# Kernel tuning notes

Measured on AMD Instinct MI355X. Metric: run time of the kernel, lower is better.

## Reference

```python
import jax, jax.numpy as jnp
import numpy as np

F, H, C = 768, 256, 16  # feature_size, lstm_hidden_size, num_classes
B, T = 256, 128         # sentences per doc, words per sentence


def lstm_scan(x, w_ih, w_hh, b, reverse=False):
    """PyTorch-convention LSTM (gates i,f,g,o). x: [B,T,D] -> (outputs [B,T,H], h_T [B,H])."""
    Hh = w_hh.shape[1]
    gx = jnp.einsum('btd,gd->btg', x, w_ih) + b      # [B,T,4H], biases fused
    gx = jnp.swapaxes(gx, 0, 1)                      # [T,B,4H]
    h0 = jnp.zeros((x.shape[0], Hh), x.dtype)
    def step(carry, g):
        h, c = carry
        g = g + h @ w_hh.T
        i, f, gg, o = jnp.split(g, 4, axis=-1)
        c = jax.nn.sigmoid(f) * c + jax.nn.sigmoid(i) * jnp.tanh(gg)
        h = jax.nn.sigmoid(o) * jnp.tanh(c)
        return (h, c), h
    (hT, _), ys = jax.lax.scan(step, (h0, h0), gx, reverse=reverse)
    return jnp.swapaxes(ys, 0, 1), hT


def setup_inputs() -> dict:
    key = jax.random.key(0)
    ks = jax.random.split(key, 16)
    s = 0.1
    return {
        'x': jax.random.normal(ks[0], (B, T, F), jnp.float32),
        'y': jax.random.randint(ks[1], (B,), 0, C),
        'mask': jnp.ones((B, T), bool),
        # BiLSTM forward / reverse directions
        'w_ih_f': jax.random.normal(ks[2], (4 * H, F)) * s,
        'w_hh_f': jax.random.normal(ks[3], (4 * H, H)) * s,
        'b_f': jax.random.normal(ks[4], (4 * H,)) * s,
        'w_ih_r': jax.random.normal(ks[5], (4 * H, F)) * s,
        'w_hh_r': jax.random.normal(ks[6], (4 * H, H)) * s,
        'b_r': jax.random.normal(ks[7], (4 * H,)) * s,
        # word_to_sent LSTM (512 -> 512)
        'w_ih_s': jax.random.normal(ks[8], (8 * H, 2 * H)) * s,
        'w_hh_s': jax.random.normal(ks[9], (8 * H, 2 * H)) * s,
        'b_s': jax.random.normal(ks[10], (8 * H,)) * s,
        # linear + CRF params
        'lin_w': jax.random.normal(ks[11], (C, 2 * H)) * s,
        'lin_b': jnp.zeros((C,)),
        'crf_start': jax.random.normal(ks[12], (C,)) * s,
        'crf_end': jax.random.normal(ks[13], (C,)) * s,
        'crf_trans': jax.random.normal(ks[14], (C, C)) * s,
    }


def reference(x, y, mask, w_ih_f, w_hh_f, b_f, w_ih_r, w_hh_r, b_r,
              w_ih_s, w_hh_s, b_s, lin_w, lin_b, crf_start, crf_end, crf_trans):
    # dropout is identity (eval-mode reference)
    out_f, _ = lstm_scan(x, w_ih_f, w_hh_f, b_f, reverse=False)
    out_r, _ = lstm_scan(x, w_ih_r, w_hh_r, b_r, reverse=True)
    h = jnp.concatenate([out_f, out_r], axis=-1)          # [B,T,2H]
    _, hT = lstm_scan(h, w_ih_s, w_hh_s, b_s)             # [B,2H] final hidden per sentence
    emissions = hT @ lin_w.T + lin_b                      # [B,C] -> CRF sequence of length B

    S = emissions.shape[0]
    # numerator: score of gold tag sequence
    num = (crf_start[y[0]] + emissions[jnp.arange(S), y].sum()
           + crf_trans[y[:-1], y[1:]].sum() + crf_end[y[-1]])
    # denominator: forward algorithm (log partition)
    def fstep(alpha, e_t):
        return jax.nn.logsumexp(alpha[:, None] + crf_trans + e_t[None, :], axis=0), None
    alpha0 = crf_start + emissions[0]
    alphaT, _ = jax.lax.scan(fstep, alpha0, emissions[1:])
    denom = jax.nn.logsumexp(alphaT + crf_end)
    return num - denom  # log-likelihood (sum reduction, single CRF batch)
```

## Files before the change

kernel.cpp:

```cpp
#include <hip/hip_runtime.h>
#include <hip/hip_bf16.h>
#include <stdint.h>


typedef __bf16 bf16_t;
typedef __bf16 bf16x8 __attribute__((ext_vector_type(8)));
typedef __bf16 bf16x4v __attribute__((ext_vector_type(4)));
typedef float f32x4 __attribute__((ext_vector_type(4)));
typedef unsigned long long u64;

#define MFMA_BF16(a, b, c) __builtin_amdgcn_mfma_f32_16x16x32_bf16((a), (b), (c), 0, 0, 0)

__device__ __forceinline__ float sigm_(float x) { return 1.f / (1.f + __expf(-x)); }
__device__ __forceinline__ float tanh_(float x) {
  x = fminf(20.f, fmaxf(-20.f, x));
  float e = __expf(-2.f * x);
  return (1.f - e) / (1.f + e);
}

__device__ __forceinline__ u64 aload8(const u64* p) {
  return __hip_atomic_load(p, __ATOMIC_RELAXED, __HIP_MEMORY_SCOPE_AGENT);
}
__device__ __forceinline__ void astore8(u64* p, u64 v) {
  __hip_atomic_store(p, v, __ATOMIC_RELAXED, __HIP_MEMORY_SCOPE_AGENT);
}

union U8 { bf16x4v v; uint2 u; };
union B8 { uint32_t u[4]; bf16x8 v; };

__global__ void zero8(u64* __restrict__ p, int n) {
  int i = blockIdx.x * 256 + threadIdx.x;
  int s = gridDim.x * 256;
  for (; i < n; i += s) p[i] = 0ull;
}

__global__ void cvt4(const float* __restrict__ in, bf16_t* __restrict__ out, int n4) {
  int i = blockIdx.x * blockDim.x + threadIdx.x;
  int stride = gridDim.x * blockDim.x;
  for (; i < n4; i += stride) {
    float4 v = ((const float4*)in)[i];
    bf16x4v o;
    o.x = (bf16_t)v.x; o.y = (bf16_t)v.y; o.z = (bf16_t)v.z; o.w = (bf16_t)v.w;
    ((bf16x4v*)out)[i] = o;
  }
}

__global__ void __launch_bounds__(256, 2)
gemm_bt(const bf16_t* __restrict__ A, const bf16_t* __restrict__ B,
        bf16_t* __restrict__ C, int M, int N, int K) {
  const int tid = threadIdx.x;
  const int w = tid >> 6, lane = tid & 63, quad = lane >> 4, l15 = lane & 15;
  const int ntiles = N >> 7;
  const int m0 = (blockIdx.x / ntiles) << 7;
  const int n0 = (blockIdx.x % ntiles) << 7;
  const int wm = (w >> 1) << 6, wn = (w & 1) << 6;

  __shared__ bf16_t As[128 * 72];
  __shared__ bf16_t Bs[128 * 72];

  const f32x4 z4 = {0.f, 0.f, 0.f, 0.f};
  f32x4 acc[4][4];
#pragma unroll
  for (int i = 0; i < 4; ++i)
#pragma unroll
    for (int j = 0; j < 4; ++j) acc[i][j] = z4;

  const int nk = K >> 6;
  for (int kt = 0; kt < nk; ++kt) {
    uint4 av[4], bv[4];
#pragma unroll
    for (int i = 0; i < 4; ++i) {
      int cid = tid + i * 256;
      int r = cid >> 3, c = cid & 7;
      av[i] = *(const uint4*)&A[(size_t)(m0 + r) * K + kt * 64 + c * 8];
      bv[i] = *(const uint4*)&B[(size_t)(n0 + r) * K + kt * 64 + c * 8];
    }
    __syncthreads();
#pragma unroll
    for (int i = 0; i < 4; ++i) {
      int cid = tid + i * 256;
      int r = cid >> 3, c = cid & 7;
      *(uint4*)&As[r * 72 + c * 8] = av[i];
      *(uint4*)&Bs[r * 72 + c * 8] = bv[i];
    }
    __syncthreads();
#pragma unroll
    for (int s = 0; s < 2; ++s) {
      bf16x8 af[4], bfr[4];
#pragma unroll
      for (int i = 0; i < 4; ++i)
        af[i] = *(const bf16x8*)&As[(wm + i * 16 + l15) * 72 + s * 32 + quad * 8];
#pragma unroll
      for (int j = 0; j < 4; ++j)
        bfr[j] = *(const bf16x8*)&Bs[(wn + j * 16 + l15) * 72 + s * 32 + quad * 8];
#pragma unroll
      for (int i = 0; i < 4; ++i)
#pragma unroll
        for (int j = 0; j < 4; ++j)
          acc[i][j] = MFMA_BF16(af[i], bfr[j], acc[i][j]);
    }
  }
#pragma unroll
  for (int i = 0; i < 4; ++i)
#pragma unroll
    for (int j = 0; j < 4; ++j)
#pragma unroll
      for (int p = 0; p < 4; ++p) {
        int row = m0 + wm + i * 16 + quad * 4 + p;
        int col = n0 + wn + j * 16 + l15;
        C[(size_t)row * N + col] = (bf16_t)acc[i][j][p];
      }
}

__global__ void __launch_bounds__(256, 1)
lstm_fr(const bf16_t* __restrict__ gx, const bf16_t* __restrict__ whh,
        const float* __restrict__ b_f, const float* __restrict__ b_r,
        bf16_t* __restrict__ h_cat, u64* __restrict__ hb,
        unsigned* __restrict__ flags) {
  const int tid = threadIdx.x;
  const int w = tid >> 6, lane = tid & 63, quad = lane >> 4, l15 = lane & 15;
  const int grp = blockIdx.x & 31;
  const int hsp = blockIdx.x >> 5;
  const int dir = grp >> 4;
  const int bg = grp & 15;
  const int rows0 = bg << 4;
  const int hid0 = hsp << 6;
  unsigned* fgrp = flags + grp * 128;
  unsigned* fmine = fgrp + hsp * 32;

  __shared__ bf16_t Ws[256 * 264];
  const bf16_t* Wg = whh + (size_t)dir * 262144;
#pragma unroll
  for (int i = 0; i < 32; ++i) {
    int id = tid + i * 256;
    int r = id >> 5, c = id & 31;
    int g = r >> 6, hh = r & 63;
    *(uint4*)&Ws[r * 264 + c * 8] =
        *(const uint4*)&Wg[(size_t)(g * 256 + hid0 + hh) * 256 + c * 8];
  }
  const float* bias = dir ? b_r : b_f;
  const int hid = hid0 + w * 16 + quad * 4;
  float br[4][4];
#pragma unroll
  for (int g = 0; g < 4; ++g)
#pragma unroll
    for (int p = 0; p < 4; ++p) br[g][p] = bias[g * 256 + hid + p];
  const int brow = rows0 + l15;
  float c4[4] = {0.f, 0.f, 0.f, 0.f};
  const f32x4 z4 = {0.f, 0.f, 0.f, 0.f};
  __syncthreads();

  for (int t = 1; t <= 128; ++t) {
    const int tt = dir ? (128 - t) : (t - 1);
    const size_t gbase = ((size_t)brow * 128 + tt) * 2048 + (size_t)dir * 1024;
    bf16x4v gp[4];
#pragma unroll
    for (int g = 0; g < 4; ++g) gp[g] = *(const bf16x4v*)&gx[gbase + g * 256 + hid];

    f32x4 acc[4];
#pragma unroll
    for (int g = 0; g < 4; ++g) acc[g] = z4;

    if (t >= 2) {
      const unsigned tgt = (unsigned)(t - 1);
      if (w == 0) {
        for (;;) {
          unsigned f = tgt;
          if (lane < 4)
            f = __hip_atomic_load(fgrp + lane * 32, __ATOMIC_RELAXED, __HIP_MEMORY_SCOPE_AGENT);
          if (__all((int)(f >= tgt))) break;
          __builtin_amdgcn_s_sleep(1);
        }
      }
      __builtin_amdgcn_s_barrier();
      __asm__ __volatile__("" ::: "memory");

      const u64* hrow = hb + (((size_t)((t & 1) ^ 1) * 2 + dir) * 256 + brow) * 128;
      u64 wv[8][4];
#pragma unroll
      for (int ks = 0; ks < 8; ++ks)
#pragma unroll
        for (int p = 0; p < 4; ++p)
          wv[ks][p] = aload8(hrow + ks * 16 + quad * 4 + p);
      unsigned miss = 0;
#pragma unroll
      for (int ks = 0; ks < 8; ++ks) {
        bool ok = ((unsigned)(wv[ks][0] >> 32) == tgt) &&
                  ((unsigned)(wv[ks][1] >> 32) == tgt) &&
                  ((unsigned)(wv[ks][2] >> 32) == tgt) &&
                  ((unsigned)(wv[ks][3] >> 32) == tgt);
        if (!__all((int)ok)) miss |= 1u << ks;
      }
      while (miss) {
        __builtin_amdgcn_s_sleep(1);
#pragma unroll
        for (int ks = 0; ks < 8; ++ks)
          if (miss & (1u << ks)) {
#pragma unroll
            for (int p = 0; p < 4; ++p)
              wv[ks][p] = aload8(hrow + ks * 16 + quad * 4 + p);
            bool ok = ((unsigned)(wv[ks][0] >> 32) == tgt) &&
                      ((unsigned)(wv[ks][1] >> 32) == tgt) &&
                      ((unsigned)(wv[ks][2] >> 32) == tgt) &&
                      ((unsigned)(wv[ks][3] >> 32) == tgt);
            if (__all((int)ok)) miss &= ~(1u << ks);
          }
      }
      __asm__ __volatile__("" ::: "memory");
#pragma unroll
      for (int ks = 0; ks < 8; ++ks) {
        B8 Bv;
#pragma unroll
        for (int p = 0; p < 4; ++p) Bv.u[p] = (uint32_t)wv[ks][p];
#pragma unroll
        for (int g = 0; g < 4; ++g) {
          bf16x8 af = *(const bf16x8*)&Ws[(g * 64 + w * 16 + l15) * 264 + ks * 32 + quad * 8];
          acc[g] = MFMA_BF16(af, Bv.v, acc[g]);
        }
      }
    }
    bf16x4v hv;
#pragma unroll
    for (int p = 0; p < 4; ++p) {
      float Pi = acc[0][p] + (float)gp[0][p] + br[0][p];
      float Pf = acc[1][p] + (float)gp[1][p] + br[1][p];
      float Pg = acc[2][p] + (float)gp[2][p] + br[2][p];
      float Po = acc[3][p] + (float)gp[3][p] + br[3][p];
      float cc = sigm_(Pf) * c4[p] + sigm_(Pi) * tanh_(Pg);
      c4[p] = cc;
      hv[p] = (bf16_t)(sigm_(Po) * tanh_(cc));
    }
    if (t < 128) {
      U8 cv; cv.v = hv;
      const u64 tag = (u64)(unsigned)t << 32;
      u64* orow = hb + (((size_t)(t & 1) * 2 + dir) * 256 + brow) * 128 + (hid >> 1);
      astore8(orow,     (u64)cv.u.x | tag);
      astore8(orow + 1, (u64)cv.u.y | tag);
      if (tid == 0)
        __hip_atomic_store(fmine, (unsigned)t, __ATOMIC_RELAXED, __HIP_MEMORY_SCOPE_AGENT);
    }
    *(bf16x4v*)&h_cat[((size_t)brow * 128 + tt) * 512 + dir * 256 + hid] = hv;
  }
}

__global__ void __launch_bounds__(256, 1)
lstm_s(const bf16_t* __restrict__ gs, const bf16_t* __restrict__ wsh,
       const float* __restrict__ b_s, float* __restrict__ hT,
       u64* __restrict__ hb, unsigned* __restrict__ flags) {
  const int tid = threadIdx.x;
  const int w = tid >> 6, lane = tid & 63, quad = lane >> 4, l15 = lane & 15;
  const int bg = blockIdx.x & 7;
  const int hsp = blockIdx.x >> 3;
  const int rows0 = bg << 5;
  const int hid0 = hsp << 5;
  const int nt = w & 1, hb2 = w >> 1;
  unsigned* fgrp = flags + bg * 512;
  unsigned* fmine = fgrp + hsp * 32;

  __shared__ bf16_t Ws[128 * 520];
#pragma unroll
  for (int i = 0; i < 32; ++i) {
    int id = tid + i * 256;
    int r = id >> 6, c = id & 63;
    int g = r >> 5, hh = r & 31;
    *(uint4*)&Ws[r * 520 + c * 8] =
        *(const uint4*)&wsh[(size_t)(g * 512 + hid0 + hh) * 512 + c * 8];
  }
  const int hid = hid0 + hb2 * 16 + quad * 4;
  float br[4][4];
#pragma unroll
  for (int g = 0; g < 4; ++g)
#pragma unroll
    for (int p = 0; p < 4; ++p) br[g][p] = b_s[g * 512 + hid + p];
  const int brow = rows0 + nt * 16 + l15;
  float c4[4] = {0.f, 0.f, 0.f, 0.f};
  const f32x4 z4 = {0.f, 0.f, 0.f, 0.f};
  __syncthreads();

  for (int t = 1; t <= 128; ++t) {
    const size_t gbase = ((size_t)brow * 128 + (t - 1)) * 2048;
    bf16x4v gp[4];
#pragma unroll
    for (int g = 0; g < 4; ++g) gp[g] = *(const bf16x4v*)&gs[gbase + g * 512 + hid];

    f32x4 acc[4];
#pragma unroll
    for (int g = 0; g < 4; ++g) acc[g] = z4;

    if (t >= 2) {
      const unsigned tgt = (unsigned)(t - 1);
      if (w == 0) {
        for (;;) {
          unsigned f = tgt;
          if (lane < 16)
            f = __hip_atomic_load(fgrp + lane * 32, __ATOMIC_RELAXED, __HIP_MEMORY_SCOPE_AGENT);
          if (__all((int)(f >= tgt))) break;
          __builtin_amdgcn_s_sleep(1);
        }
      }
      __builtin_amdgcn_s_barrier();
      __asm__ __volatile__("" ::: "memory");

      const u64* hrow = hb + ((size_t)((t & 1) ^ 1) * 256 + brow) * 256;
#pragma unroll
      for (int kb = 0; kb < 2; ++kb) {
        u64 wv[8][4];
#pragma unroll
        for (int i = 0; i < 8; ++i)
#pragma unroll
          for (int p = 0; p < 4; ++p)
            wv[i][p] = aload8(hrow + (kb * 8 + i) * 16 + quad * 4 + p);
        unsigned miss = 0;
#pragma unroll
        for (int i = 0; i < 8; ++i) {
          bool ok = ((unsigned)(wv[i][0] >> 32) == tgt) &&
                    ((unsigned)(wv[i][1] >> 32) == tgt) &&
                    ((unsigned)(wv[i][2] >> 32) == tgt) &&
                    ((unsigned)(wv[i][3] >> 32) == tgt);
          if (!__all((int)ok)) miss |= 1u << i;
        }
        while (miss) {
          __builtin_amdgcn_s_sleep(1);
#pragma unroll
          for (int i = 0; i < 8; ++i)
            if (miss & (1u << i)) {
#pragma unroll
              for (int p = 0; p < 4; ++p)
                wv[i][p] = aload8(hrow + (kb * 8 + i) * 16 + quad * 4 + p);
              bool ok = ((unsigned)(wv[i][0] >> 32) == tgt) &&
                        ((unsigned)(wv[i][1] >> 32) == tgt) &&
                        ((unsigned)(wv[i][2] >> 32) == tgt) &&
                        ((unsigned)(wv[i][3] >> 32) == tgt);
              if (__all((int)ok)) miss &= ~(1u << i);
            }
        }
        __asm__ __volatile__("" ::: "memory");
#pragma unroll
        for (int i = 0; i < 8; ++i) {
          const int ks = kb * 8 + i;
          B8 Bv;
#pragma unroll
          for (int p = 0; p < 4; ++p) Bv.u[p] = (uint32_t)wv[i][p];
#pragma unroll
          for (int g = 0; g < 4; ++g) {
            bf16x8 af = *(const bf16x8*)&Ws[(g * 32 + hb2 * 16 + l15) * 520 + ks * 32 + quad * 8];
            acc[g] = MFMA_BF16(af, Bv.v, acc[g]);
          }
        }
      }
    }
    bf16x4v hv;
    float hf[4];
#pragma unroll
    for (int p = 0; p < 4; ++p) {
      float Pi = acc[0][p] + (float)gp[0][p] + br[0][p];
      float Pf = acc[1][p] + (float)gp[1][p] + br[1][p];
      float Pg = acc[2][p] + (float)gp[2][p] + br[2][p];
      float Po = acc[3][p] + (float)gp[3][p] + br[3][p];
      float cc = sigm_(Pf) * c4[p] + sigm_(Pi) * tanh_(Pg);
      c4[p] = cc;
      hf[p] = sigm_(Po) * tanh_(cc);
      hv[p] = (bf16_t)hf[p];
    }
    if (t < 128) {
      U8 cv; cv.v = hv;
      const u64 tag = (u64)(unsigned)t << 32;
      u64* orow = hb + ((size_t)(t & 1) * 256 + brow) * 256 + (hid >> 1);
      astore8(orow,     (u64)cv.u.x | tag);
      astore8(orow + 1, (u64)cv.u.y | tag);
      if (tid == 0)
        __hip_atomic_store(fmine, (unsigned)t, __ATOMIC_RELAXED, __HIP_MEMORY_SCOPE_AGENT);
    } else {
      *(float4*)&hT[(size_t)brow * 512 + hid] = make_float4(hf[0], hf[1], hf[2], hf[3]);
    }
  }
}

__global__ void emis_k(const float* __restrict__ hT, const float* __restrict__ lin_w,
                       const float* __restrict__ lin_b, float* __restrict__ em) {
  const int idx = blockIdx.x * 256 + threadIdx.x;
  const int s = idx >> 4, c = idx & 15;
  const float4* h4 = (const float4*)(hT + (size_t)s * 512);
  const float4* w4 = (const float4*)(lin_w + (size_t)c * 512);
  float acc = lin_b[c];
  for (int k = 0; k < 128; ++k) {
    float4 a = h4[k], b = w4[k];
    acc += a.x * b.x + a.y * b.y + a.z * b.z + a.w * b.w;
  }
  em[idx] = acc;
}

__global__ void crf_k(const float* __restrict__ em, const int* __restrict__ y,
                      const float* __restrict__ cs, const float* __restrict__ ce,
                      const float* __restrict__ tr, float* __restrict__ out) {
  __shared__ float alpha[16];
  __shared__ float trs[256];
  const int lane = threadIdx.x;
  const int i = lane & 15, jg = lane >> 4;

  for (int k = lane; k < 256; k += 64) trs[k] = tr[k];
  __syncthreads();

  float np = 0.f;
  for (int s = lane; s < 256; s += 64) np += em[s * 16 + y[s]];
  for (int s = lane + 1; s < 256; s += 64) np += trs[y[s - 1] * 16 + y[s]];
#pragma unroll
  for (int off = 32; off > 0; off >>= 1) np += __shfl_down(np, off, 64);

  if (lane < 16) alpha[lane] = cs[lane] + em[lane];
  __syncthreads();

  for (int s = 1; s < 256; ++s) {
    const float* e = em + s * 16;
    float v[4];
#pragma unroll
    for (int jj = 0; jj < 4; ++jj) v[jj] = alpha[i] + trs[i * 16 + (jj * 4 + jg)];
    float res[4];
#pragma unroll
    for (int jj = 0; jj < 4; ++jj) {
      float m = v[jj];
      m = fmaxf(m, __shfl_xor(m, 1, 64));
      m = fmaxf(m, __shfl_xor(m, 2, 64));
      m = fmaxf(m, __shfl_xor(m, 4, 64));
      m = fmaxf(m, __shfl_xor(m, 8, 64));
      float ex = __expf(v[jj] - m);
      ex += __shfl_xor(ex, 1, 64);
      ex += __shfl_xor(ex, 2, 64);
      ex += __shfl_xor(ex, 4, 64);
      ex += __shfl_xor(ex, 8, 64);
      res[jj] = m + __logf(ex) + e[jj * 4 + jg];
    }
#pragma unroll
    for (int jj = 0; jj < 4; ++jj)
      if (i == 0) alpha[jj * 4 + jg] = res[jj];
  }

  float v = (lane < 16) ? (alpha[lane] + ce[lane]) : -3.0e38f;
  float m = v;
#pragma unroll
  for (int off = 32; off > 0; off >>= 1) m = fmaxf(m, __shfl_xor(m, off, 64));
  float ex = __expf(v - m);
#pragma unroll
  for (int off = 32; off > 0; off >>= 1) ex += __shfl_xor(ex, off, 64);
  float denom = m + __logf(ex);

  if (lane == 0) {
    float num = np + cs[y[0]] + ce[y[255]];
    out[0] = num - denom;
  }
}

extern "C" void kernel_launch(void* const* d_in, const int* in_sizes, int n_in,
                              void* d_out, int out_size, void* d_ws, size_t ws_size,
                              hipStream_t stream) {
  const float* x = (const float*)d_in[0];
  const int* y = (const int*)d_in[1];
  const float* w_ih_f = (const float*)d_in[3];
  const float* w_hh_f = (const float*)d_in[4];
  const float* b_f = (const float*)d_in[5];
  const float* w_ih_r = (const float*)d_in[6];
  const float* w_hh_r = (const float*)d_in[7];
  const float* b_r = (const float*)d_in[8];
  const float* w_ih_s = (const float*)d_in[9];
  const float* w_hh_s = (const float*)d_in[10];
  const float* b_s = (const float*)d_in[11];
  const float* lin_w = (const float*)d_in[12];
  const float* lin_b = (const float*)d_in[13];
  const float* crf_s = (const float*)d_in[14];
  const float* crf_e = (const float*)d_in[15];
  const float* crf_t = (const float*)d_in[16];

  char* ws = (char*)d_ws;
  size_t off = 0;
  auto take = [&](size_t bytes) {
    void* p = ws + off;
    off += (bytes + 255) & ~(size_t)255;
    return p;
  };
  bf16_t* Wx  = (bf16_t*)take((size_t)2048 * 768 * 2);
  bf16_t* Whh = (bf16_t*)take((size_t)2 * 1024 * 256 * 2);
  bf16_t* Wsi = (bf16_t*)take((size_t)2048 * 512 * 2);
  bf16_t* Wsh = (bf16_t*)take((size_t)2048 * 512 * 2);
  bf16_t* gx  = (bf16_t*)take((size_t)32768 * 2048 * 2);
  bf16_t* xb  = (bf16_t*)take((size_t)32768 * 768 * 2);
  float* hT   = (float*)take((size_t)256 * 512 * 4);
  float* em   = (float*)take((size_t)4096 * 4);
  bf16_t* gs = gx;
  bf16_t* hcat = xb;
  char* tail = (char*)xb + 33554432;
  u64* hb_fr = (u64*)tail;
  u64* hb_s  = (u64*)(tail + 1048576);
  unsigned* flags_fr = (unsigned*)(tail + 2097152);
  unsigned* flags_s  = flags_fr + 4096;
  (void)ws_size; (void)in_sizes; (void)n_in; (void)out_size;

  cvt4<<<2048, 256, 0, stream>>>(x, xb, 32768 * 768 / 4);
  cvt4<<<64, 256, 0, stream>>>(w_ih_f, Wx, 786432 / 4);
  cvt4<<<64, 256, 0, stream>>>(w_ih_r, Wx + 786432, 786432 / 4);
  cvt4<<<32, 256, 0, stream>>>(w_hh_f, Whh, 262144 / 4);
  cvt4<<<32, 256, 0, stream>>>(w_hh_r, Whh + 262144, 262144 / 4);
  cvt4<<<64, 256, 0, stream>>>(w_ih_s, Wsi, 1048576 / 4);
  cvt4<<<64, 256, 0, stream>>>(w_hh_s, Wsh, 1048576 / 4);

  gemm_bt<<<4096, 256, 0, stream>>>(xb, Wx, gx, 32768, 2048, 768);

  zero8<<<512, 256, 0, stream>>>(hb_fr, 266240);

  lstm_fr<<<128, 256, 0, stream>>>(gx, Whh, b_f, b_r, hcat, hb_fr, flags_fr);

  gemm_bt<<<4096, 256, 0, stream>>>(hcat, Wsi, gs, 32768, 2048, 512);

  lstm_s<<<128, 256, 0, stream>>>(gs, Wsh, b_s, hT, hb_s, flags_s);

  emis_k<<<16, 256, 0, stream>>>(hT, lin_w, lin_b, em);
  crf_k<<<1, 64, 0, stream>>>(em, y, crf_s, crf_e, crf_t, (float*)d_out);
}
```

Baseline: 3.041 ms.

## Run each BiLSTM batch group in one 1024-thread block with LDS h exchange

```diff
diff --git a/kernel.cpp b/kernel.cpp
--- a/kernel.cpp
+++ b/kernel.cpp
@@ -112,34 +112,29 @@
       }
 }
 
-__global__ void __launch_bounds__(256, 1)
+__global__ void __launch_bounds__(1024, 1)
 lstm_fr(const bf16_t* __restrict__ gx, const bf16_t* __restrict__ whh,
         const float* __restrict__ b_f, const float* __restrict__ b_r,
-        bf16_t* __restrict__ h_cat, u64* __restrict__ hb,
-        unsigned* __restrict__ flags) {
+        bf16_t* __restrict__ h_cat) {
   const int tid = threadIdx.x;
   const int w = tid >> 6, lane = tid & 63, quad = lane >> 4, l15 = lane & 15;
-  const int grp = blockIdx.x & 31;
-  const int hsp = blockIdx.x >> 5;
-  const int dir = grp >> 4;
-  const int bg = grp & 15;
+  const int dir = blockIdx.x >> 4;
+  const int bg = blockIdx.x & 15;
   const int rows0 = bg << 4;
-  const int hid0 = hsp << 6;
-  unsigned* fgrp = flags + grp * 128;
-  unsigned* fmine = fgrp + hsp * 32;
-
-  __shared__ bf16_t Ws[256 * 264];
-  const bf16_t* Wg = whh + (size_t)dir * 262144;
-#pragma unroll
-  for (int i = 0; i < 32; ++i) {
-    int id = tid + i * 256;
-    int r = id >> 5, c = id & 31;
-    int g = r >> 6, hh = r & 63;
-    *(uint4*)&Ws[r * 264 + c * 8] =
-        *(const uint4*)&Wg[(size_t)(g * 256 + hid0 + hh) * 256 + c * 8];
-  }
+
+  __shared__ bf16_t hx[2][16 * 264];
+
+  const bf16_t* Wd = whh + (size_t)dir * 262144;
+  bf16x8 wf[4][8];
+#pragma unroll
+  for (int g = 0; g < 4; ++g)
+#pragma unroll
+    for (int kc = 0; kc < 8; ++kc)
+      wf[g][kc] = *(const bf16x8*)
+          &Wd[(size_t)(g * 256 + w * 16 + l15) * 256 + kc * 32 + quad * 8];
+
   const float* bias = dir ? b_r : b_f;
-  const int hid = hid0 + w * 16 + quad * 4;
+  const int hid = w * 16 + quad * 4;
   float br[4][4];
 #pragma unroll
   for (int g = 0; g < 4; ++g)
@@ -148,98 +143,63 @@
   const int brow = rows0 + l15;
   float c4[4] = {0.f, 0.f, 0.f, 0.f};
   const f32x4 z4 = {0.f, 0.f, 0.f, 0.f};
-  __syncthreads();
+
+  bf16x4v gpc[4];
+  {
+    const int tt0 = dir ? 127 : 0;
+    const size_t gb = ((size_t)brow * 128 + tt0) * 2048 + (size_t)dir * 1024;
+#pragma unroll
+    for (int g = 0; g < 4; ++g) gpc[g] = *(const bf16x4v*)&gx[gb + g * 256 + hid];
+  }
 
   for (int t = 1; t <= 128; ++t) {
-    const int tt = dir ? (128 - t) : (t - 1);
-    const size_t gbase = ((size_t)brow * 128 + tt) * 2048 + (size_t)dir * 1024;
-    bf16x4v gp[4];
-#pragma unroll
-    for (int g = 0; g < 4; ++g) gp[g] = *(const bf16x4v*)&gx[gbase + g * 256 + hid];
+    bf16x4v gpn[4];
+    if (t < 128) {
+      const int ttn = dir ? (128 - (t + 1)) : t;
+      const size_t gb = ((size_t)brow * 128 + ttn) * 2048 + (size_t)dir * 1024;
+#pragma unroll
+      for (int g = 0; g < 4; ++g) gpn[g] = *(const bf16x4v*)&gx[gb + g * 256 + hid];
+    }
 
     f32x4 acc[4];
 #pragma unroll
     for (int g = 0; g < 4; ++g) acc[g] = z4;
 
     if (t >= 2) {
-      const unsigned tgt = (unsigned)(t - 1);
-      if (w == 0) {
-        for (;;) {
-          unsigned f = tgt;
-          if (lane < 4)
-            f = __hip_atomic_load(fgrp + lane * 32, __ATOMIC_RELAXED, __HIP_MEMORY_SCOPE_AGENT);
-          if (__all((int)(f >= tgt))) break;
-          __builtin_amdgcn_s_sleep(1);
-        }
+      const bf16_t* hs = hx[(t & 1) ^ 1];
+#pragma unroll
+      for (int kc = 0; kc < 8; ++kc) {
+        bf16x8 bfv = *(const bf16x8*)&hs[l15 * 264 + kc * 32 + quad * 8];
+#pragma unroll
+        for (int g = 0; g < 4; ++g) acc[g] = MFMA_BF16(wf[g][kc], bfv, acc[g]);
       }
-      __builtin_amdgcn_s_barrier();
-      __asm__ __volatile__("" ::: "memory");
-
-      const u64* hrow = hb + (((size_t)((t & 1) ^ 1) * 2 + dir) * 256 + brow) * 128;
-      u64 wv[8][4];
-#pragma unroll
-      for (int ks = 0; ks < 8; ++ks)
-#pragma unroll
-        for (int p = 0; p < 4; ++p)
-          wv[ks][p] = aload8(hrow + ks * 16 + quad * 4 + p);
-      unsigned miss = 0;
-#pragma unroll
-      for (int ks = 0; ks < 8; ++ks) {
-        bool ok = ((unsigned)(wv[ks][0] >> 32) == tgt) &&
-                  ((unsigned)(wv[ks][1] >> 32) == tgt) &&
-                  ((unsigned)(wv[ks][2] >> 32) == tgt) &&
-                  ((unsigned)(wv[ks][3] >> 32) == tgt);
-        if (!__all((int)ok)) miss |= 1u << ks;
-      }
-      while (miss) {
-        __builtin_amdgcn_s_sleep(1);
-#pragma unroll
-        for (int ks = 0; ks < 8; ++ks)
-          if (miss & (1u << ks)) {
-#pragma unroll
-            for (int p = 0; p < 4; ++p)
-              wv[ks][p] = aload8(hrow + ks * 16 + quad * 4 + p);
-            bool ok = ((unsigned)(wv[ks][0] >> 32) == tgt) &&
-                      ((unsigned)(wv[ks][1] >> 32) == tgt) &&
-                      ((unsigned)(wv[ks][2] >> 32) == tgt) &&
-                      ((unsigned)(wv[ks][3] >> 32) == tgt);
-            if (__all((int)ok)) miss &= ~(1u << ks);
-          }
-      }
-      __asm__ __volatile__("" ::: "memory");
-#pragma unroll
-      for (int ks = 0; ks < 8; ++ks) {
-        B8 Bv;
-#pragma unroll
-        for (int p = 0; p < 4; ++p) Bv.u[p] = (uint32_t)wv[ks][p];
-#pragma unroll
-        for (int g = 0; g < 4; ++g) {
-          bf16x8 af = *(const bf16x8*)&Ws[(g * 64 + w * 16 + l15) * 264 + ks * 32 + quad * 8];
-          acc[g] = MFMA_BF16(af, Bv.v, acc[g]);
-        }
-      }
-    }
+    }
+
+    const int ttc = dir ? (128 - t) : (t - 1);
     bf16x4v hv;
 #pragma unroll
     for (int p = 0; p < 4; ++p) {
-      float Pi = acc[0][p] + (float)gp[0][p] + br[0][p];
-      float Pf = acc[1][p] + (float)gp[1][p] + br[1][p];
-      float Pg = acc[2][p] + (float)gp[2][p] + br[2][p];
-      float Po = acc[3][p] + (float)gp[3][p] + br[3][p];
+      float Pi = acc[0][p] + (float)gpc[0][p] + br[0][p];
+      float Pf = acc[1][p] + (float)gpc[1][p] + br[1][p];
+      float Pg = acc[2][p] + (float)gpc[2][p] + br[2][p];
+      float Po = acc[3][p] + (float)gpc[3][p] + br[3][p];
       float cc = sigm_(Pf) * c4[p] + sigm_(Pi) * tanh_(Pg);
       c4[p] = cc;
       hv[p] = (bf16_t)(sigm_(Po) * tanh_(cc));
     }
+    *(bf16x4v*)&h_cat[((size_t)brow * 128 + ttc) * 512 + dir * 256 + hid] = hv;
     if (t < 128) {
       U8 cv; cv.v = hv;
-      const u64 tag = (u64)(unsigned)t << 32;
-      u64* orow = hb + (((size_t)(t & 1) * 2 + dir) * 256 + brow) * 128 + (hid >> 1);
-      astore8(orow,     (u64)cv.u.x | tag);
-      astore8(orow + 1, (u64)cv.u.y | tag);
-      if (tid == 0)
-        __hip_atomic_store(fmine, (unsigned)t, __ATOMIC_RELAXED, __HIP_MEMORY_SCOPE_AGENT);
-    }
-    *(bf16x4v*)&h_cat[((size_t)brow * 128 + tt) * 512 + dir * 256 + hid] = hv;
+      *(uint2*)&hx[t & 1][l15 * 264 + hid] = cv.u;
+    }
+    __asm__ __volatile__("s_waitcnt lgkmcnt(0)" ::: "memory");
+    __builtin_amdgcn_s_barrier();
+    __asm__ __volatile__("" ::: "memory");
+
+    if (t < 128) {
+#pragma unroll
+      for (int g = 0; g < 4; ++g) gpc[g] = gpn[g];
+    }
   }
 }
 
@@ -488,10 +448,8 @@
   bf16_t* gs = gx;
   bf16_t* hcat = xb;
   char* tail = (char*)xb + 33554432;
-  u64* hb_fr = (u64*)tail;
-  u64* hb_s  = (u64*)(tail + 1048576);
-  unsigned* flags_fr = (unsigned*)(tail + 2097152);
-  unsigned* flags_s  = flags_fr + 4096;
+  u64* hb_s  = (u64*)tail;
+  unsigned* flags_s = (unsigned*)(tail + 1048576);
   (void)ws_size; (void)in_sizes; (void)n_in; (void)out_size;
 
   cvt4<<<2048, 256, 0, stream>>>(x, xb, 32768 * 768 / 4);
@@ -504,9 +462,9 @@
 
   gemm_bt<<<4096, 256, 0, stream>>>(xb, Wx, gx, 32768, 2048, 768);
 
-  zero8<<<512, 256, 0, stream>>>(hb_fr, 266240);
-
-  lstm_fr<<<128, 256, 0, stream>>>(gx, Whh, b_f, b_r, hcat, hb_fr, flags_fr);
+  zero8<<<512, 256, 0, stream>>>(hb_s, 133120);
+
+  lstm_fr<<<32, 1024, 0, stream>>>(gx, Whh, b_f, b_r, hcat);
 
   gemm_bt<<<4096, 256, 0, stream>>>(hcat, Wsi, gs, 32768, 2048, 512);
 
```

Measured after the change: 3.651 ms. 20.1% more time.
